# Performance work log

Hardware: AMD Instinct MI355X
Metric: run time of the kernel (lower is better)

Reference implementation:

```python
import jax, jax.numpy as jnp
import numpy as np

HID = 256
NP_ = 100
KS = 3
EPS = 1e-5


def setup_inputs() -> dict:
    key = jax.random.key(0)
    k1, k2, k3, k4 = jax.random.split(key, 4)
    B = 1024
    f = jax.random.normal(k1, (B, NP_, HID), dtype=jnp.float32)
    k = jax.random.normal(k2, (B, NP_, HID), dtype=jnp.float32)
    W_lin = jax.random.normal(k3, (HID, NP_ * KS), dtype=jnp.float32) / np.sqrt(HID)
    b_lin = jax.random.normal(k4, (NP_ * KS,), dtype=jnp.float32) * 0.01
    gamma = jnp.ones((HID,), dtype=jnp.float32)
    beta = jnp.zeros((HID,), dtype=jnp.float32)
    return {"f": f, "k": k, "W_lin": W_lin, "b_lin": b_lin, "gamma": gamma, "beta": beta}


def reference(f, k, W_lin, b_lin, gamma, beta):
    B, P, L = k.shape  # [B, 100, 256]
    # dynamic conv weights: [B, out=100, in=100, T=3]
    w = (jnp.einsum('bph,ho->bpo', f, W_lin) + b_lin).reshape(B, P, P, KS)
    # 'same' padding for kernel 3 -> pad 1 each side along L
    kp = jnp.pad(k, ((0, 0), (0, 0), (1, 1)))
    # shifted views: [B, in, L, T] (cross-correlation, as torch conv1d)
    ks = jnp.stack([kp[:, :, t:t + L] for t in range(KS)], axis=-1)
    out = jnp.einsum('boct,bclt->bol', w, ks)  # [B, 100, 256]
    # LayerNorm over last dim
    mu = jnp.mean(out, axis=-1, keepdims=True)
    var = jnp.mean((out - mu) ** 2, axis=-1, keepdims=True)
    return (out - mu) / jnp.sqrt(var + EPS) * gamma + beta
```

## Files before the change

kernel.cpp:

```cpp
#include <hip/hip_runtime.h>
#include <hip/hip_bf16.h>

#define HID   256
#define NP    100
#define KSZ   3
#define NPKS  (NP*KSZ)
#define K2PAD 384
#define N1T   24
#define PC    104
#define KTROWS 258
#define KT_ELEMS (KTROWS*PC + 80)
#define WS_PITCH 40
#define WS_ELEMS (112*WS_PITCH)

using bf16x8 = __attribute__((ext_vector_type(8))) short;
using f32x4  = __attribute__((ext_vector_type(4))) float;

__device__ __forceinline__ short f2bf(float x) {
    __hip_bfloat16 h = __float2bfloat16(x);
    return __builtin_bit_cast(short, h);
}

__global__ void dyconv_prep(const float* __restrict__ W_lin,
                            const float* __restrict__ b_lin,
                            short* __restrict__ W2f,
                            float* __restrict__ b2f) {
    int gid = blockIdx.x * blockDim.x + threadIdx.x;
    int lane = gid & 63;
    int ent  = gid >> 6;
    int kt = ent / N1T;
    int nt = ent % N1T;
    int n  = nt*16 + (lane & 15);
    int t  = n >> 7;
    int c  = n & 127;
    int k0 = kt*32 + ((lane >> 4) << 3);
    short vals[8];
#pragma unroll
    for (int j = 0; j < 8; ++j) {
        float v = (c < NP) ? W_lin[(k0 + j) * NPKS + c*KSZ + t] : 0.0f;
        vals[j] = f2bf(v);
    }
    *reinterpret_cast<bf16x8*>(&W2f[(size_t)gid * 8]) =
        *reinterpret_cast<bf16x8*>(vals);
    if (gid < K2PAD) {
        int tt = gid >> 7, cc = gid & 127;
        b2f[gid] = (cc < NP) ? b_lin[cc*KSZ + tt] : 0.0f;
    }
}

__global__ __launch_bounds__(256, 4)
void dyconv_gemm1(const float* __restrict__ f, const short* __restrict__ W2f,
                  const float* __restrict__ b2f, short* __restrict__ w2, int Mrows) {
    __shared__ short wlds[2][16*512];
    const int tid = threadIdx.x, wave = tid>>6, lane = tid&63, lg = lane>>4, li = lane&15;
    const int r0 = blockIdx.x * 128;

    bf16x8 a1[2][8];
#pragma unroll
    for (int mi = 0; mi < 2; ++mi) {
        int myr = r0 + (wave*2 + mi)*16 + li; if (myr > Mrows-1) myr = Mrows-1;
        const float* frow = f + (size_t)myr * HID + lg*8;
#pragma unroll
        for (int kt = 0; kt < 8; ++kt) {
            float4 u = *reinterpret_cast<const float4*>(frow + kt*32);
            float4 v = *reinterpret_cast<const float4*>(frow + kt*32 + 4);
            short tmp[8] = {f2bf(u.x),f2bf(u.y),f2bf(u.z),f2bf(u.w),
                            f2bf(v.x),f2bf(v.y),f2bf(v.z),f2bf(v.w)};
            a1[mi][kt] = *reinterpret_cast<bf16x8*>(tmp);
        }
    }

#define STAGE(BUF, C) { _Pragma("unroll") for (int i = 0; i < 4; ++i) { \
        int fi = wave*4 + i; \
        int ntl = fi >> 3, kt = fi & 7; \
        int nt = (C)*2 + ntl; \
        const short* gsrc = &W2f[(((size_t)(kt*N1T + nt))*64 + lane)*8]; \
        __builtin_amdgcn_global_load_lds( \
            (const __attribute__((address_space(1))) unsigned int*)gsrc, \
            (__attribute__((address_space(3))) unsigned int*)&wlds[BUF][fi*512], \
            16, 0, 0); } }

    const int prow0 = lg*4;

    STAGE(0, 0)
    __syncthreads();

#pragma unroll 1
    for (int c = 0; c < 12; ++c) {
        if (c < 11) STAGE((c+1)&1, c+1)

        const short* lbase = wlds[c&1];
        f32x4 acc[2][2];
#pragma unroll
        for (int mi = 0; mi < 2; ++mi)
#pragma unroll
            for (int i = 0; i < 2; ++i) acc[mi][i] = (f32x4){0.f,0.f,0.f,0.f};

#pragma unroll
        for (int ntl = 0; ntl < 2; ++ntl) {
#pragma unroll
            for (int kt = 0; kt < 8; ++kt) {
                bf16x8 bfr = *reinterpret_cast<const bf16x8*>(
                    lbase + (ntl*8 + kt)*512 + lane*8);
                acc[0][ntl] = __builtin_amdgcn_mfma_f32_16x16x32_bf16(
                    a1[0][kt], bfr, acc[0][ntl], 0,0,0);
                acc[1][ntl] = __builtin_amdgcn_mfma_f32_16x16x32_bf16(
                    a1[1][kt], bfr, acc[1][ntl], 0,0,0);
            }
        }

        float bias[2];
#pragma unroll
        for (int ntl = 0; ntl < 2; ++ntl) bias[ntl] = b2f[(c*2 + ntl)*16 + li];

#pragma unroll
        for (int mi = 0; mi < 2; ++mi) {
#pragma unroll
            for (int r = 0; r < 4; ++r) {
                int gr = r0 + (wave*2 + mi)*16 + prow0 + r;
                if (gr < Mrows) {
                    int bb = gr / NP, p = gr % NP;
                    short* wrow = w2 + ((size_t)bb*12*NP + p)*32;
#pragma unroll
                    for (int ntl = 0; ntl < 2; ++ntl) {
                        int nt = c*2 + ntl;
                        wrow[(size_t)(nt>>1)*NP*32 + (nt&1)*16 + li] =
                            f2bf(acc[mi][ntl][r] + bias[ntl]);
                    }
                }
            }
        }
        __syncthreads();
    }
#undef STAGE
}

__global__ __launch_bounds__(256, 2)
void dyconv_conv(const float* __restrict__ k, const short* __restrict__ w2,
                 const float* __restrict__ gamma, const float* __restrict__ beta,
                 float* __restrict__ out) {
    __shared__ short kT[KT_ELEMS];
    float* lnbuf = reinterpret_cast<float*>(kT);

    const int b = blockIdx.x, tid = threadIdx.x;
    const int wave = tid>>6, lane = tid&63, lg = lane>>4, li = lane&15;

    if (tid < 52) {
        *reinterpret_cast<unsigned int*>(&kT[tid*2]) = 0u;
        *reinterpret_cast<unsigned int*>(&kT[257*PC + tid*2]) = 0u;
    }
    *reinterpret_cast<unsigned long long*>(&kT[(tid+1)*PC + 100]) = 0ull;
    if (tid < 20)
        *reinterpret_cast<unsigned long long*>(&kT[KTROWS*PC + tid*4]) = 0ull;

    const float* kb = k + (size_t)b * (NP*HID);
    for (int u = tid; u < (NP/2)*HID; u += 256) {
        int c2 = u >> 8;
        int l  = u & 255;
        int c  = c2*2;
        float v0 = kb[(size_t)c*HID + l];
        float v1 = kb[(size_t)(c+1)*HID + l];
        unsigned int pk = (unsigned int)(unsigned short)f2bf(v0)
                        | ((unsigned int)(unsigned short)f2bf(v1) << 16);
        *reinterpret_cast<unsigned int*>(&kT[(l+1)*PC + c]) = pk;
    }

    f32x4 acc2[7][4];
#pragma unroll
    for (int mt = 0; mt < 7; ++mt)
#pragma unroll
        for (int j = 0; j < 4; ++j) acc2[mt][j] = (f32x4){0.f,0.f,0.f,0.f};

    const short* wb = w2 + (size_t)b * 12 * NP * 32;
    const short* wp[7];
#pragma unroll
    for (int mt = 0; mt < 7; ++mt) {
        int p = mt*16 + li; if (p > NP-1) p = NP-1;
        wp[mt] = wb + (size_t)p*32 + lg*8;
    }

    __syncthreads();

    bf16x8 a2[7], a2n[7];
#pragma unroll
    for (int mt = 0; mt < 7; ++mt)
        a2[mt] = *reinterpret_cast<const bf16x8*>(wp[mt]);

#pragma unroll
    for (int kc = 0; kc < 12; ++kc) {
        if (kc < 11) {
#pragma unroll
            for (int mt = 0; mt < 7; ++mt)
                a2n[mt] = *reinterpret_cast<const bf16x8*>(wp[mt] + (size_t)(kc+1)*NP*32);
        }
        int k2 = kc*32 + lg*8;
        int t  = k2 >> 7, c = k2 & 127;
#pragma unroll
        for (int j = 0; j < 4; ++j) {
            int l = (wave*4 + j)*16 + li;
            bf16x8 b2v = *reinterpret_cast<const bf16x8*>(&kT[(l + t)*PC + c]);
#pragma unroll
            for (int mt = 0; mt < 7; ++mt)
                acc2[mt][j] = __builtin_amdgcn_mfma_f32_16x16x32_bf16(
                    a2[mt], b2v, acc2[mt][j], 0,0,0);
        }
#pragma unroll
        for (int mt = 0; mt < 7; ++mt) a2[mt] = a2n[mt];
    }

    __syncthreads();

    float* psum  = lnbuf;
    float* mrstd = lnbuf + 4*112*2;
#pragma unroll
    for (int mt = 0; mt < 7; ++mt) {
#pragma unroll
        for (int r = 0; r < 4; ++r) {
            float s1 = 0.f, s2 = 0.f;
#pragma unroll
            for (int j = 0; j < 4; ++j) {
                float v = acc2[mt][j][r];
                s1 += v; s2 += v*v;
            }
#pragma unroll
            for (int m = 1; m < 16; m <<= 1) {
                s1 += __shfl_xor(s1, m, 64);
                s2 += __shfl_xor(s2, m, 64);
            }
            if (li == 0) {
                int p = mt*16 + lg*4 + r;
                psum[(wave*112 + p)*2 + 0] = s1;
                psum[(wave*112 + p)*2 + 1] = s2;
            }
        }
    }
    __syncthreads();
    if (tid < 112) {
        float S1 = 0.f, S2 = 0.f;
#pragma unroll
        for (int w2i = 0; w2i < 4; ++w2i) {
            S1 += psum[(w2i*112 + tid)*2 + 0];
            S2 += psum[(w2i*112 + tid)*2 + 1];
        }
        float mean = S1 * (1.0f/HID);
        float var  = S2 * (1.0f/HID) - mean*mean;
        mrstd[tid*2 + 0] = mean;
        mrstd[tid*2 + 1] = rsqrtf(var + 1e-5f);
    }
    __syncthreads();

    float* ob = out + (size_t)b * (NP*HID);
#pragma unroll
    for (int j = 0; j < 4; ++j) {
        int l = (wave*4 + j)*16 + li;
        float g  = gamma[l];
        float be = beta[l];
#pragma unroll
        for (int mt = 0; mt < 7; ++mt) {
#pragma unroll
            for (int r = 0; r < 4; ++r) {
                int p = mt*16 + lg*4 + r;
                if (p < NP) {
                    float mean = mrstd[p*2], rstd = mrstd[p*2 + 1];
                    ob[p*HID + l] = (acc2[mt][j][r] - mean)*rstd*g + be;
                }
            }
        }
    }
}

__global__ __launch_bounds__(256)
void dyconv_main(const float* __restrict__ f, const float* __restrict__ k,
                 const short* __restrict__ W2f, const float* __restrict__ b2f,
                 const float* __restrict__ gamma, const float* __restrict__ beta,
                 float* __restrict__ out) {
    __shared__ short kT[KT_ELEMS];
    __shared__ short wS[WS_ELEMS];
    float* lnbuf = reinterpret_cast<float*>(wS);
    const int b = blockIdx.x, tid = threadIdx.x;
    const int wave = tid>>6, lane = tid&63, lg = lane>>4, li = lane&15;
    for (int i = tid; i < KT_ELEMS/8; i += 256)
        reinterpret_cast<int4*>(kT)[i] = make_int4(0,0,0,0);
    __syncthreads();
    const float* kb = k + (size_t)b * (NP*HID);
    for (int idx = tid; idx < NP*HID; idx += 256) {
        int c = idx >> 8, l = idx & 255;
        kT[(l+1)*PC + c] = f2bf(kb[idx]);
    }
    const float* fb = f + (size_t)b * (NP*HID);
    const int nmy = (wave < 3) ? 2 : 1;
    bf16x8 a1[2][8];
#pragma unroll
    for (int mi = 0; mi < 2; ++mi) {
        if (mi < nmy) {
            int mt = wave + 4*mi;
            int p  = mt*16 + li; if (p > NP-1) p = NP-1;
            const float* rowp = fb + (size_t)p * HID + lg*8;
#pragma unroll
            for (int kt = 0; kt < 8; ++kt) {
                float4 u = *reinterpret_cast<const float4*>(rowp + kt*32);
                float4 v = *reinterpret_cast<const float4*>(rowp + kt*32 + 4);
                short tmp[8] = {f2bf(u.x),f2bf(u.y),f2bf(u.z),f2bf(u.w),
                                f2bf(v.x),f2bf(v.y),f2bf(v.z),f2bf(v.w)};
                a1[mi][kt] = *reinterpret_cast<bf16x8*>(tmp);
            }
        }
    }
    f32x4 acc2[7][4];
#pragma unroll
    for (int mt = 0; mt < 7; ++mt)
#pragma unroll
        for (int j = 0; j < 4; ++j) acc2[mt][j] = (f32x4){0.f,0.f,0.f,0.f};
    __syncthreads();
    for (int kc = 0; kc < 12; ++kc) {
        f32x4 acc1[2][2];
#pragma unroll
        for (int mi = 0; mi < 2; ++mi)
#pragma unroll
            for (int n = 0; n < 2; ++n) acc1[mi][n] = (f32x4){0.f,0.f,0.f,0.f};
#pragma unroll
        for (int kt = 0; kt < 8; ++kt) {
            bf16x8 b1[2];
#pragma unroll
            for (int ntl = 0; ntl < 2; ++ntl) {
                int NT = kc*2 + ntl;
                b1[ntl] = *reinterpret_cast<const bf16x8*>(
                    &W2f[(((size_t)kt*N1T + NT)*64 + lane)*8]);
            }
#pragma unroll
            for (int mi = 0; mi < 2; ++mi) {
                if (mi < nmy) {
                    acc1[mi][0] = __builtin_amdgcn_mfma_f32_16x16x32_bf16(
                        a1[mi][kt], b1[0], acc1[mi][0], 0,0,0);
                    acc1[mi][1] = __builtin_amdgcn_mfma_f32_16x16x32_bf16(
                        a1[mi][kt], b1[1], acc1[mi][1], 0,0,0);
                }
            }
        }
#pragma unroll
        for (int mi = 0; mi < 2; ++mi) {
            if (mi < nmy) {
                int mt = wave + 4*mi;
#pragma unroll
                for (int ntl = 0; ntl < 2; ++ntl) {
                    int col  = ntl*16 + li;
                    float bias = b2f[kc*32 + col];
#pragma unroll
                    for (int r = 0; r < 4; ++r) {
                        int row = mt*16 + lg*4 + r;
                        wS[row*WS_PITCH + col] = f2bf(acc1[mi][ntl][r] + bias);
                    }
                }
            }
        }
        __syncthreads();
        bf16x8 a2[7];
#pragma unroll
        for (int mt = 0; mt < 7; ++mt)
            a2[mt] = *reinterpret_cast<const bf16x8*>(&wS[(mt*16 + li)*WS_PITCH + lg*8]);
        int k2 = kc*32 + lg*8;
        int t  = k2 >> 7, c = k2 & 127;
#pragma unroll
        for (int j = 0; j < 4; ++j) {
            int l = (wave*4 + j)*16 + li;
            bf16x8 b2v = *reinterpret_cast<const bf16x8*>(&kT[(l + t)*PC + c]);
#pragma unroll
            for (int mt = 0; mt < 7; ++mt)
                acc2[mt][j] = __builtin_amdgcn_mfma_f32_16x16x32_bf16(
                    a2[mt], b2v, acc2[mt][j], 0,0,0);
        }
        __syncthreads();
    }
    float* psum  = lnbuf;
    float* mrstd = lnbuf + 4*112*2;
#pragma unroll
    for (int mt = 0; mt < 7; ++mt) {
#pragma unroll
        for (int r = 0; r < 4; ++r) {
            float s1 = 0.f, s2 = 0.f;
#pragma unroll
            for (int j = 0; j < 4; ++j) {
                float v = acc2[mt][j][r];
                s1 += v; s2 += v*v;
            }
#pragma unroll
            for (int m = 1; m < 16; m <<= 1) {
                s1 += __shfl_xor(s1, m, 64);
                s2 += __shfl_xor(s2, m, 64);
            }
            if (li == 0) {
                int p = mt*16 + lg*4 + r;
                psum[(wave*112 + p)*2 + 0] = s1;
                psum[(wave*112 + p)*2 + 1] = s2;
            }
        }
    }
    __syncthreads();
    if (tid < 112) {
        float S1 = 0.f, S2 = 0.f;
#pragma unroll
        for (int w2i = 0; w2i < 4; ++w2i) {
            S1 += psum[(w2i*112 + tid)*2 + 0];
            S2 += psum[(w2i*112 + tid)*2 + 1];
        }
        float mean = S1 * (1.0f/HID);
        float var  = S2 * (1.0f/HID) - mean*mean;
        mrstd[tid*2 + 0] = mean;
        mrstd[tid*2 + 1] = rsqrtf(var + 1e-5f);
    }
    __syncthreads();
    float* ob = out + (size_t)b * (NP*HID);
#pragma unroll
    for (int j = 0; j < 4; ++j) {
        int l = (wave*4 + j)*16 + li;
        float g  = gamma[l];
        float be = beta[l];
#pragma unroll
        for (int mt = 0; mt < 7; ++mt) {
#pragma unroll
            for (int r = 0; r < 4; ++r) {
                int p = mt*16 + lg*4 + r;
                if (p < NP) {
                    float mean = mrstd[p*2], rstd = mrstd[p*2 + 1];
                    ob[p*HID + l] = (acc2[mt][j][r] - mean)*rstd*g + be;
                }
            }
        }
    }
}

extern "C" void kernel_launch(void* const* d_in, const int* in_sizes, int n_in,
                              void* d_out, int out_size, void* d_ws, size_t ws_size,
                              hipStream_t stream) {
    const float* f     = (const float*)d_in[0];
    const float* k     = (const float*)d_in[1];
    const float* W_lin = (const float*)d_in[2];
    const float* b_lin = (const float*)d_in[3];
    const float* gamma = (const float*)d_in[4];
    const float* beta  = (const float*)d_in[5];
    float* out = (float*)d_out;

    short* W2f = (short*)d_ws;
    float* b2f = (float*)((char*)d_ws + 196608);
    const size_t off_w2 = 198144;
    const int B = in_sizes[0] / (NP*HID);
    const int Mrows = B * NP;
    const size_t need = off_w2 + (size_t)B * 12 * NP * 32 * 2;

    dyconv_prep<<<48, 256, 0, stream>>>(W_lin, b_lin, W2f, b2f);

    if (ws_size >= need) {
        short* w2 = (short*)((char*)d_ws + off_w2);
        dyconv_gemm1<<<(Mrows + 127)/128, 256, 0, stream>>>(f, W2f, b2f, w2, Mrows);
        dyconv_conv<<<B, 256, 0, stream>>>(k, w2, gamma, beta, out);
    } else {
        dyconv_main<<<B, 256, 0, stream>>>(f, k, W2f, b2f, gamma, beta, out);
    }
}
```

Measured before the change: 149.1 us.

## Split conv row tiles into two passes to cut registers and raise occupancy

The conv kernel's 7 M-tiles of accumulators are now processed in two passes (4 tiles, then 3), each doing its own LayerNorm and store, which shrinks the live accumulator set. Launch bounds go from 2 to 3 blocks per SM. The LDS partial-sum buffer shrinks and the cross-wave reduction moves to shared-memory atomics. In exchange, the K-tile LDS reads are repeated for the second pass and extra barriers are added.

```diff
diff --git a/kernel.cpp b/kernel.cpp
--- a/kernel.cpp
+++ b/kernel.cpp
@@ -9,9 +9,9 @@
 #define N1T   24
 #define PC    104
 #define KTROWS 258
-#define KT_ELEMS (KTROWS*PC + 80)
 #define WS_PITCH 40
 #define WS_ELEMS (112*WS_PITCH)
+#define KT_ELEMS_FB (KTROWS*PC + 80)
 
 using bf16x8 = __attribute__((ext_vector_type(8))) short;
 using f32x4  = __attribute__((ext_vector_type(4))) float;
@@ -135,12 +135,105 @@
 #undef STAGE
 }
 
-__global__ __launch_bounds__(256, 2)
+template<int NMT, int MTB>
+__device__ __forceinline__ void conv_pass(
+    const short* __restrict__ wb, const short* __restrict__ kT,
+    float* __restrict__ psumA,
+    const float* __restrict__ gamma, const float* __restrict__ beta,
+    float* __restrict__ ob, int wave, int lg, int li)
+{
+    f32x4 acc[NMT][4];
+#pragma unroll
+    for (int mt = 0; mt < NMT; ++mt)
+#pragma unroll
+        for (int j = 0; j < 4; ++j) acc[mt][j] = (f32x4){0.f,0.f,0.f,0.f};
+
+    const short* wp[NMT];
+#pragma unroll
+    for (int mt = 0; mt < NMT; ++mt) {
+        int p = (MTB + mt)*16 + li; if (p > NP-1) p = NP-1;
+        wp[mt] = wb + (size_t)p*32 + lg*8;
+    }
+
+    bf16x8 a2[NMT], a2n[NMT];
+#pragma unroll
+    for (int mt = 0; mt < NMT; ++mt)
+        a2[mt] = *reinterpret_cast<const bf16x8*>(wp[mt]);
+
+#pragma unroll
+    for (int kc = 0; kc < 12; ++kc) {
+        if (kc < 11) {
+#pragma unroll
+            for (int mt = 0; mt < NMT; ++mt)
+                a2n[mt] = *reinterpret_cast<const bf16x8*>(wp[mt] + (size_t)(kc+1)*NP*32);
+        }
+        int k2 = kc*32 + lg*8;
+        int t  = k2 >> 7, c = k2 & 127;
+#pragma unroll
+        for (int j = 0; j < 4; ++j) {
+            int l = (wave*4 + j)*16 + li;
+            bf16x8 b2v = *reinterpret_cast<const bf16x8*>(&kT[(l + t)*PC + c]);
+#pragma unroll
+            for (int mt = 0; mt < NMT; ++mt)
+                acc[mt][j] = __builtin_amdgcn_mfma_f32_16x16x32_bf16(
+                    a2[mt], b2v, acc[mt][j], 0,0,0);
+        }
+#pragma unroll
+        for (int mt = 0; mt < NMT; ++mt) a2[mt] = a2n[mt];
+    }
+
+#pragma unroll
+    for (int mt = 0; mt < NMT; ++mt) {
+#pragma unroll
+        for (int r = 0; r < 4; ++r) {
+            float s1 = 0.f, s2 = 0.f;
+#pragma unroll
+            for (int j = 0; j < 4; ++j) {
+                float v = acc[mt][j][r];
+                s1 += v; s2 += v*v;
+            }
+#pragma unroll
+            for (int m = 1; m < 16; m <<= 1) {
+                s1 += __shfl_xor(s1, m, 64);
+                s2 += __shfl_xor(s2, m, 64);
+            }
+            if (li == 0) {
+                int rl = mt*16 + lg*4 + r;
+                atomicAdd(&psumA[rl*2 + 0], s1);
+                atomicAdd(&psumA[rl*2 + 1], s2);
+            }
+        }
+    }
+    __syncthreads();
+
+#pragma unroll
+    for (int j = 0; j < 4; ++j) {
+        int l = (wave*4 + j)*16 + li;
+        float g  = gamma[l];
+        float be = beta[l];
+#pragma unroll
+        for (int mt = 0; mt < NMT; ++mt) {
+#pragma unroll
+            for (int r = 0; r < 4; ++r) {
+                int rl = mt*16 + lg*4 + r;
+                int p  = MTB*16 + rl;
+                if (p < NP) {
+                    float S1 = psumA[rl*2], S2 = psumA[rl*2 + 1];
+                    float mean = S1 * (1.0f/HID);
+                    float rstd = rsqrtf(S2 * (1.0f/HID) - mean*mean + 1e-5f);
+                    ob[p*HID + l] = (acc[mt][j][r] - mean)*rstd*g + be;
+                }
+            }
+        }
+    }
+}
+
+__global__ __launch_bounds__(256, 3)
 void dyconv_conv(const float* __restrict__ k, const short* __restrict__ w2,
                  const float* __restrict__ gamma, const float* __restrict__ beta,
                  float* __restrict__ out) {
-    __shared__ short kT[KT_ELEMS];
-    float* lnbuf = reinterpret_cast<float*>(kT);
+    __shared__ short kT[KTROWS*PC];
+    __shared__ float psumA[64*2];
 
     const int b = blockIdx.x, tid = threadIdx.x;
     const int wave = tid>>6, lane = tid&63, lg = lane>>4, li = lane&15;
@@ -150,8 +243,7 @@
         *reinterpret_cast<unsigned int*>(&kT[257*PC + tid*2]) = 0u;
     }
     *reinterpret_cast<unsigned long long*>(&kT[(tid+1)*PC + 100]) = 0ull;
-    if (tid < 20)
-        *reinterpret_cast<unsigned long long*>(&kT[KTROWS*PC + tid*4]) = 0ull;
+    if (tid < 128) psumA[tid] = 0.f;
 
     const float* kb = k + (size_t)b * (NP*HID);
     for (int u = tid; u < (NP/2)*HID; u += 256) {
@@ -165,108 +257,18 @@
         *reinterpret_cast<unsigned int*>(&kT[(l+1)*PC + c]) = pk;
     }
 
-    f32x4 acc2[7][4];
-#pragma unroll
-    for (int mt = 0; mt < 7; ++mt)
-#pragma unroll
-        for (int j = 0; j < 4; ++j) acc2[mt][j] = (f32x4){0.f,0.f,0.f,0.f};
-
     const short* wb = w2 + (size_t)b * 12 * NP * 32;
-    const short* wp[7];
-#pragma unroll
-    for (int mt = 0; mt < 7; ++mt) {
-        int p = mt*16 + li; if (p > NP-1) p = NP-1;
-        wp[mt] = wb + (size_t)p*32 + lg*8;
-    }
-
-    __syncthreads();
-
-    bf16x8 a2[7], a2n[7];
-#pragma unroll
-    for (int mt = 0; mt < 7; ++mt)
-        a2[mt] = *reinterpret_cast<const bf16x8*>(wp[mt]);
-
-#pragma unroll
-    for (int kc = 0; kc < 12; ++kc) {
-        if (kc < 11) {
-#pragma unroll
-            for (int mt = 0; mt < 7; ++mt)
-                a2n[mt] = *reinterpret_cast<const bf16x8*>(wp[mt] + (size_t)(kc+1)*NP*32);
-        }
-        int k2 = kc*32 + lg*8;
-        int t  = k2 >> 7, c = k2 & 127;
-#pragma unroll
-        for (int j = 0; j < 4; ++j) {
-            int l = (wave*4 + j)*16 + li;
-            bf16x8 b2v = *reinterpret_cast<const bf16x8*>(&kT[(l + t)*PC + c]);
-#pragma unroll
-            for (int mt = 0; mt < 7; ++mt)
-                acc2[mt][j] = __builtin_amdgcn_mfma_f32_16x16x32_bf16(
-                    a2[mt], b2v, acc2[mt][j], 0,0,0);
-        }
-#pragma unroll
-        for (int mt = 0; mt < 7; ++mt) a2[mt] = a2n[mt];
-    }
-
-    __syncthreads();
-
-    float* psum  = lnbuf;
-    float* mrstd = lnbuf + 4*112*2;
-#pragma unroll
-    for (int mt = 0; mt < 7; ++mt) {
-#pragma unroll
-        for (int r = 0; r < 4; ++r) {
-            float s1 = 0.f, s2 = 0.f;
-#pragma unroll
-            for (int j = 0; j < 4; ++j) {
-                float v = acc2[mt][j][r];
-                s1 += v; s2 += v*v;
-            }
-#pragma unroll
-            for (int m = 1; m < 16; m <<= 1) {
-                s1 += __shfl_xor(s1, m, 64);
-                s2 += __shfl_xor(s2, m, 64);
-            }
-            if (li == 0) {
-                int p = mt*16 + lg*4 + r;
-                psum[(wave*112 + p)*2 + 0] = s1;
-                psum[(wave*112 + p)*2 + 1] = s2;
-            }
-        }
-    }
-    __syncthreads();
-    if (tid < 112) {
-        float S1 = 0.f, S2 = 0.f;
-#pragma unroll
-        for (int w2i = 0; w2i < 4; ++w2i) {
-            S1 += psum[(w2i*112 + tid)*2 + 0];
-            S2 += psum[(w2i*112 + tid)*2 + 1];
-        }
-        float mean = S1 * (1.0f/HID);
-        float var  = S2 * (1.0f/HID) - mean*mean;
-        mrstd[tid*2 + 0] = mean;
-        mrstd[tid*2 + 1] = rsqrtf(var + 1e-5f);
-    }
-    __syncthreads();
-
     float* ob = out + (size_t)b * (NP*HID);
-#pragma unroll
-    for (int j = 0; j < 4; ++j) {
-        int l = (wave*4 + j)*16 + li;
-        float g  = gamma[l];
-        float be = beta[l];
-#pragma unroll
-        for (int mt = 0; mt < 7; ++mt) {
-#pragma unroll
-            for (int r = 0; r < 4; ++r) {
-                int p = mt*16 + lg*4 + r;
-                if (p < NP) {
-                    float mean = mrstd[p*2], rstd = mrstd[p*2 + 1];
-                    ob[p*HID + l] = (acc2[mt][j][r] - mean)*rstd*g + be;
-                }
-            }
-        }
-    }
+
+    __syncthreads();
+
+    conv_pass<4, 0>(wb, kT, psumA, gamma, beta, ob, wave, lg, li);
+
+    __syncthreads();
+    if (tid < 128) psumA[tid] = 0.f;
+    __syncthreads();
+
+    conv_pass<3, 4>(wb, kT, psumA, gamma, beta, ob, wave, lg, li);
 }
 
 __global__ __launch_bounds__(256)
@@ -274,12 +276,12 @@
                  const short* __restrict__ W2f, const float* __restrict__ b2f,
                  const float* __restrict__ gamma, const float* __restrict__ beta,
                  float* __restrict__ out) {
-    __shared__ short kT[KT_ELEMS];
+    __shared__ short kT[KT_ELEMS_FB];
     __shared__ short wS[WS_ELEMS];
     float* lnbuf = reinterpret_cast<float*>(wS);
     const int b = blockIdx.x, tid = threadIdx.x;
     const int wave = tid>>6, lane = tid&63, lg = lane>>4, li = lane&15;
-    for (int i = tid; i < KT_ELEMS/8; i += 256)
+    for (int i = tid; i < KT_ELEMS_FB/8; i += 256)
         reinterpret_cast<int4*>(kT)[i] = make_int4(0,0,0,0);
     __syncthreads();
     const float* kb = k + (size_t)b * (NP*HID);
```

New measurement: 144.2 us. -3.3%, faster.

## Stage dynamic conv weights into LDS via double-buffered global_load_lds

Applied to the files above, without the earlier changes.

The conv kernel no longer has each wave load its own A-operand weight fragments from global memory into registers. Each k-chunk of the per-batch weights is now copied cooperatively into a double-buffered LDS area with direct global-to-LDS loads, and the MFMA operands are read from LDS, with a barrier per chunk. This removes redundant global reads across the four waves and frees registers used for prefetching. The cost is more LDS traffic, 12 barriers, and a non-unrolled k loop. The LayerNorm scratch buffer now aliases the new weight buffer, and the k-transpose load loop gets an unroll hint.

```diff
diff --git a/kernel.cpp b/kernel.cpp
--- a/kernel.cpp
+++ b/kernel.cpp
@@ -9,9 +9,9 @@
 #define N1T   24
 #define PC    104
 #define KTROWS 258
-#define KT_ELEMS (KTROWS*PC + 80)
 #define WS_PITCH 40
 #define WS_ELEMS (112*WS_PITCH)
+#define KT_ELEMS_FB (KTROWS*PC + 80)
 
 using bf16x8 = __attribute__((ext_vector_type(8))) short;
 using f32x4  = __attribute__((ext_vector_type(4))) float;
@@ -139,8 +139,9 @@
 void dyconv_conv(const float* __restrict__ k, const short* __restrict__ w2,
                  const float* __restrict__ gamma, const float* __restrict__ beta,
                  float* __restrict__ out) {
-    __shared__ short kT[KT_ELEMS];
-    float* lnbuf = reinterpret_cast<float*>(kT);
+    __shared__ short kT[KTROWS*PC];
+    __shared__ __align__(16) short w2b[2][3584];
+    float* lnbuf = reinterpret_cast<float*>(w2b);
 
     const int b = blockIdx.x, tid = threadIdx.x;
     const int wave = tid>>6, lane = tid&63, lg = lane>>4, li = lane&15;
@@ -150,10 +151,9 @@
         *reinterpret_cast<unsigned int*>(&kT[257*PC + tid*2]) = 0u;
     }
     *reinterpret_cast<unsigned long long*>(&kT[(tid+1)*PC + 100]) = 0ull;
-    if (tid < 20)
-        *reinterpret_cast<unsigned long long*>(&kT[KTROWS*PC + tid*4]) = 0ull;
 
     const float* kb = k + (size_t)b * (NP*HID);
+#pragma unroll 5
     for (int u = tid; u < (NP/2)*HID; u += 256) {
         int c2 = u >> 8;
         int l  = u & 255;
@@ -165,33 +165,34 @@
         *reinterpret_cast<unsigned int*>(&kT[(l+1)*PC + c]) = pk;
     }
 
+    const short* wkc = w2 + (size_t)b * 12 * NP * 32;
+
+#define STAGEW(BUF, KC) { for (int i = tid; i < 400; i += 256) { \
+        const short* gsrc = wkc + (size_t)(KC)*NP*32 + (size_t)i*8; \
+        __builtin_amdgcn_global_load_lds( \
+            (const __attribute__((address_space(1))) unsigned int*)gsrc, \
+            (__attribute__((address_space(3))) unsigned int*)&w2b[BUF][i*8], \
+            16, 0, 0); } }
+
     f32x4 acc2[7][4];
 #pragma unroll
     for (int mt = 0; mt < 7; ++mt)
 #pragma unroll
         for (int j = 0; j < 4; ++j) acc2[mt][j] = (f32x4){0.f,0.f,0.f,0.f};
 
-    const short* wb = w2 + (size_t)b * 12 * NP * 32;
-    const short* wp[7];
-#pragma unroll
-    for (int mt = 0; mt < 7; ++mt) {
-        int p = mt*16 + li; if (p > NP-1) p = NP-1;
-        wp[mt] = wb + (size_t)p*32 + lg*8;
-    }
-
-    __syncthreads();
-
-    bf16x8 a2[7], a2n[7];
-#pragma unroll
-    for (int mt = 0; mt < 7; ++mt)
-        a2[mt] = *reinterpret_cast<const bf16x8*>(wp[mt]);
-
-#pragma unroll
+    STAGEW(0, 0)
+    __syncthreads();
+
+#pragma unroll 1
     for (int kc = 0; kc < 12; ++kc) {
-        if (kc < 11) {
-#pragma unroll
-            for (int mt = 0; mt < 7; ++mt)
-                a2n[mt] = *reinterpret_cast<const bf16x8*>(wp[mt] + (size_t)(kc+1)*NP*32);
+        if (kc < 11) STAGEW((kc+1)&1, kc+1)
+
+        const short* wbuf = w2b[kc&1];
+        bf16x8 a2[7];
+#pragma unroll
+        for (int mt = 0; mt < 7; ++mt) {
+            int p = mt*16 + li; if (p > NP-1) p = NP-1;
+            a2[mt] = *reinterpret_cast<const bf16x8*>(&wbuf[p*32 + lg*8]);
         }
         int k2 = kc*32 + lg*8;
         int t  = k2 >> 7, c = k2 & 127;
@@ -204,11 +205,9 @@
                 acc2[mt][j] = __builtin_amdgcn_mfma_f32_16x16x32_bf16(
                     a2[mt], b2v, acc2[mt][j], 0,0,0);
         }
-#pragma unroll
-        for (int mt = 0; mt < 7; ++mt) a2[mt] = a2n[mt];
-    }
-
-    __syncthreads();
+        __syncthreads();
+    }
+#undef STAGEW
 
     float* psum  = lnbuf;
     float* mrstd = lnbuf + 4*112*2;
@@ -274,12 +273,12 @@
                  const short* __restrict__ W2f, const float* __restrict__ b2f,
                  const float* __restrict__ gamma, const float* __restrict__ beta,
                  float* __restrict__ out) {
-    __shared__ short kT[KT_ELEMS];
+    __shared__ short kT[KT_ELEMS_FB];
     __shared__ short wS[WS_ELEMS];
     float* lnbuf = reinterpret_cast<float*>(wS);
     const int b = blockIdx.x, tid = threadIdx.x;
     const int wave = tid>>6, lane = tid&63, lg = lane>>4, li = lane&15;
-    for (int i = tid; i < KT_ELEMS/8; i += 256)
+    for (int i = tid; i < KT_ELEMS_FB/8; i += 256)
         reinterpret_cast<int4*>(kT)[i] = make_int4(0,0,0,0);
     __syncthreads();
     const float* kb = k + (size_t)b * (NP*HID);
```

Result: faster. 145.4 us (-2.5%).
